# Kernel tuning notes

Hardware: AMD Instinct MI355X
Metric: run time of the kernel (lower is better)

The kernel has to match this reference:

```python
import math
import jax, jax.numpy as jnp
import numpy as np

H, W = 720, 1280
N_GRIDS = 7
CTX = 24          # ARM context pixels
MASK = 9          # causal neighborhood mask size
GAIN = 16.0       # encoder_gain
T = 0.3           # soft_round_temperature
LOG_SCALE_CLAMP = 13.8155
SIZES = [(math.ceil(H / 2 ** i), math.ceil(W / 2 ** i)) for i in range(N_GRIDS)]


def _ctx_offsets():
    # CTX closest strictly-causal pixels (raster order before center) in a 9x9 mask
    c = MASK // 2
    cand = []
    for idx in range((MASK * MASK) // 2):  # indices 0..39 are causal
        r, col = divmod(idx, MASK)
        cand.append(((r - c) ** 2 + (col - c) ** 2, idx, r, col))
    cand.sort()
    sel = sorted(cand[:CTX], key=lambda t: t[1])
    return [(r, col) for _, _, r, col in sel]

OFFSETS = _ctx_offsets()


def softround(x, t):
    fl = jnp.floor(x)
    delta = x - fl - 0.5
    return fl + 0.5 * jnp.tanh(delta / t) / jnp.tanh(0.5 / t) + 0.5


def laplace_cdf(x, mu, scale):
    d = x - mu
    return 0.5 - 0.5 * jnp.sign(d) * jnp.expm1(-jnp.abs(d) / scale)


def get_neighbor(lat):
    # lat: (1,1,h,w) -> (h*w, CTX) causal context, zero padded borders
    h, w = lat.shape[2], lat.shape[3]
    pad = MASK // 2
    p = jnp.pad(lat[0, 0], pad)
    ctx = jnp.stack([p[r:r + h, c:c + w] for (r, c) in OFFSETS], axis=-1)
    return ctx.reshape(-1, CTX)


def depthwise_conv_same(x, k):
    # x: (1,C,h,w), k: (kh,kw) shared across channels
    ch = x.shape[1]
    xr = x.reshape(ch, 1, x.shape[2], x.shape[3])
    y = jax.lax.conv_general_dilated(xr, k[None, None], (1, 1), 'SAME',
                                     dimension_numbers=('NCHW', 'OIHW', 'NCHW'))
    return y.reshape(1, ch, y.shape[2], y.shape[3])


def depthwise_convT2(x, k):
    # stride-2 transposed conv, kernel (8,8) shared across channels
    ch = x.shape[1]
    xr = x.reshape(ch, 1, x.shape[2], x.shape[3])
    y = jax.lax.conv_transpose(xr, k[None, None], (2, 2), 'VALID',
                               dimension_numbers=('NCHW', 'OIHW', 'NCHW'))
    return y.reshape(1, ch, y.shape[2], y.shape[3])


def conv2d(x, w, b):
    y = jax.lax.conv_general_dilated(x, w, (1, 1), 'SAME',
                                     dimension_numbers=('NCHW', 'OIHW', 'NCHW'))
    return y + b[None, :, None, None]


def setup_inputs() -> dict:
    key = jax.random.key(0)
    ks = jax.random.split(key, 24)
    inp = {}
    for i, (h, w) in enumerate(SIZES):
        inp[f'latent{i}'] = jax.random.normal(ks[i], (1, 1, h, w), jnp.float32) * 0.05
    s = 1.0 / math.sqrt(CTX)
    inp['arm_w0'] = jax.random.normal(ks[7], (CTX, 24), jnp.float32) * s
    inp['arm_b0'] = jnp.zeros((24,), jnp.float32)
    inp['arm_w1'] = jax.random.normal(ks[8], (24, 24), jnp.float32) * s
    inp['arm_b1'] = jnp.zeros((24,), jnp.float32)
    inp['arm_wout'] = jax.random.normal(ks[9], (24, 2), jnp.float32) * s
    inp['arm_bout'] = jnp.zeros((2,), jnp.float32)
    inp['pre_kernels'] = jax.random.normal(ks[10], (N_GRIDS - 1, 7, 7), jnp.float32) * 0.05 + \
        jnp.zeros((N_GRIDS - 1, 7, 7), jnp.float32).at[:, 3, 3].set(1.0)
    inp['ups_kernels'] = jax.random.normal(ks[11], (N_GRIDS - 1, 8, 8), jnp.float32) * 0.05 + 0.25
    inp['syn_w0'] = jax.random.normal(ks[12], (48, 7, 1, 1), jnp.float32) * (1.0 / math.sqrt(7))
    inp['syn_b0'] = jnp.zeros((48,), jnp.float32)
    inp['syn_w1'] = jax.random.normal(ks[13], (6, 48, 1, 1), jnp.float32) * (1.0 / math.sqrt(48))
    inp['syn_b1'] = jnp.zeros((6,), jnp.float32)
    inp['syn_w2'] = jax.random.normal(ks[14], (6, 6, 3, 3), jnp.float32) * (1.0 / math.sqrt(54))
    inp['syn_b2'] = jnp.zeros((6,), jnp.float32)
    inp['syn_w3'] = jax.random.normal(ks[15], (6, 6, 3, 3), jnp.float32) * (1.0 / math.sqrt(54))
    inp['syn_b3'] = jnp.zeros((6,), jnp.float32)
    return inp


def _forward(latent0, latent1, latent2, latent3, latent4, latent5, latent6,
             arm_w0, arm_b0, arm_w1, arm_b1, arm_wout, arm_bout,
             pre_kernels, ups_kernels,
             syn_w0, syn_b0, syn_w1, syn_b1, syn_w2, syn_b2, syn_w3, syn_b3):
    lats = [latent0, latent1, latent2, latent3, latent4, latent5, latent6]
    # --- quantize (softround, deterministic) ---
    flat = jnp.concatenate([l.reshape(-1) for l in lats]) * GAIN
    q = softround(flat, T)
    dec, cnt = [], 0
    for l in lats:
        n = l.size
        dec.append(q[cnt:cnt + n].reshape(l.shape))
        cnt += n
    # --- causal neighbor gather + tiny ARM MLP ---
    ctx = jnp.concatenate([get_neighbor(d) for d in dec], axis=0)   # (N, CTX)
    flat_lat = jnp.concatenate([d.reshape(-1) for d in dec])        # (N,)
    h0 = jax.nn.relu(ctx @ arm_w0 + arm_b0)
    h1 = jax.nn.relu(h0 @ arm_w1 + arm_b1)
    out = h1 @ arm_wout + arm_bout                                  # (N, 2)
    mu_f = out[:, 0]
    scale_f = jnp.exp(-0.5 * jnp.clip(out[:, 1], -LOG_SCALE_CLAMP, LOG_SCALE_CLAMP))
    # --- Laplace-CDF rate ---
    proba = jnp.clip(laplace_cdf(flat_lat + 0.5, mu_f, scale_f)
                     - laplace_cdf(flat_lat - 0.5, mu_f, scale_f), 2.0 ** -16, None)
    rate = -jnp.log2(proba)
    # --- upsampling: coarsest -> finest, smooth + x2 transpose conv + concat ---
    x = dec[-1]
    for step, i in enumerate(range(N_GRIDS - 2, -1, -1)):
        x = depthwise_conv_same(x, pre_kernels[step])
        x = depthwise_convT2(x, ups_kernels[step])
        ht, wt = SIZES[i]
        x = x[:, :, 3:3 + ht, 3:3 + wt]
        x = jnp.concatenate([dec[i], x], axis=1)
    # --- synthesis: 48-1-linear-relu, 6-1-linear-none, 6-3-residual-relu, 6-3-residual-none ---
    s0 = jax.nn.relu(conv2d(x, syn_w0, syn_b0))
    s1 = conv2d(s0, syn_w1, syn_b1)
    s2 = jax.nn.relu(conv2d(s1, syn_w2, syn_b2) + s1)
    s3 = conv2d(s2, syn_w3, syn_b3) + s2
    mu = s3[:, :3]
    scale = jnp.exp(-0.5 * jnp.clip(s3[:, 3:6], -LOG_SCALE_CLAMP, LOG_SCALE_CLAMP))
    latent_bpd = rate.sum() / (H * W * 3)
    return mu, scale, rate, latent_bpd


def reference(latent0, latent1, latent2, latent3, latent4, latent5, latent6,
              arm_w0, arm_b0, arm_w1, arm_b1, arm_wout, arm_bout,
              pre_kernels, ups_kernels,
              syn_w0, syn_b0, syn_w1, syn_b1, syn_w2, syn_b2, syn_w3, syn_b3):
    return _forward(latent0, latent1, latent2, latent3, latent4, latent5, latent6,
                    arm_w0, arm_b0, arm_w1, arm_b1, arm_wout, arm_bout,
                    pre_kernels, ups_kernels,
                    syn_w0, syn_b0, syn_w1, syn_b1, syn_w2, syn_b2, syn_w3, syn_b3)
```

## Files before the change

### kernel.cpp

```cpp
#include <hip/hip_runtime.h>

#define NLAT 1228760
#define RATE_OFF 5529600
#define BPD_OFF 6758360
#define NB_ARM 4800
#define LSC 13.8155f

typedef float v2f __attribute__((ext_vector_type(2)));

static __device__ const int d_GOFF[8] = {0,921600,1152000,1209600,1224000,1227600,1228520,1228760};
static __device__ const int d_GW[7]   = {1280,640,320,160,80,40,20};
static __device__ const int d_XOFF[7] = {0,6451200,7833600,8121600,8179200,8190000,8191840};

#define S1_OFF   9574480
#define BSUM_OFF 15104080

static __device__ const int d_DR[24] = {-4,-3,-3,-3,-3,-3,-2,-2,-2,-2,-2,-2,-2,-1,-1,-1,-1,-1,-1,-1, 0, 0, 0, 0};
static __device__ const int d_DC[24] = { 0,-2,-1, 0, 1, 2,-3,-2,-1, 0, 1, 2, 3,-3,-2,-1, 0, 1, 2, 3,-4,-3,-2,-1};

__device__ __forceinline__ float softround_f(float x) {
    float fl = floorf(x);
    float d = x - fl - 0.5f;
    float t = __expf(d * 6.6666667f);
    float th = __fdividef(t - 1.0f, t + 1.0f);
    return fl + 0.5f + 0.53699369f * th;
}

__global__ __launch_bounds__(256) void k_quant(
    const float* __restrict__ l0, const float* __restrict__ l1,
    const float* __restrict__ l2, const float* __restrict__ l3,
    const float* __restrict__ l4, const float* __restrict__ l5,
    const float* __restrict__ l6, float* __restrict__ ws)
{
    int t = blockIdx.x*256 + threadIdx.x;
    if (t >= NLAT) return;
    int g = 0;
    #pragma unroll
    for (int i = 1; i < 7; ++i) if (t >= d_GOFF[i]) g = i;
    int local = t - d_GOFF[g];
    const float* lp = l0;
    if      (g==1) lp=l1; else if (g==2) lp=l2; else if (g==3) lp=l3;
    else if (g==4) lp=l4; else if (g==5) lp=l5; else if (g==6) lp=l6;
    ws[d_XOFF[g] + local] = softround_f(lp[local] * 16.0f);
}

__device__ __forceinline__ void arm_body(
    const float* __restrict__ ws,
    const float* __restrict__ w0, const float* __restrict__ b0,
    const float* __restrict__ w1, const float* __restrict__ b1,
    const float* __restrict__ wo, const float* __restrict__ bo,
    float* __restrict__ out_rate, float* __restrict__ bsum, int ablk)
{
    int t = ablk*256 + threadIdx.x;
    float rate = 0.0f;
    if (t < NLAT) {
        int g = 0;
        #pragma unroll
        for (int i = 1; i < 7; ++i) if (t >= d_GOFF[i]) g = i;
        int local = t - d_GOFF[g];
        int w = d_GW[g];
        int y = (int)((unsigned)local / (unsigned)w);
        int x = local - y*w;
        const float* __restrict__ q = ws + d_XOFF[g];

        float ctx[24];
        if (y >= 4 && x >= 4 && x < w-4) {
            const float* base = q + y*w + x;
            #pragma unroll
            for (int k = 0; k < 24; ++k)
                ctx[k] = base[d_DR[k]*w + d_DC[k]];
        } else {
            #pragma unroll
            for (int k = 0; k < 24; ++k) {
                int yy = y + d_DR[k];
                int xx = x + d_DC[k];
                float v = 0.0f;
                if (yy >= 0 && (unsigned)xx < (unsigned)w) v = q[yy*w + xx];
                ctx[k] = v;
            }
        }

        const v2f* __restrict__ w0v = (const v2f*)w0;
        const v2f* __restrict__ w1v = (const v2f*)w1;
        const v2f* __restrict__ b0v = (const v2f*)b0;
        const v2f* __restrict__ b1v = (const v2f*)b1;
        const v2f* __restrict__ wov = (const v2f*)wo;
        const v2f z2 = {0.0f, 0.0f};

        v2f h0[12];
        #pragma unroll
        for (int j = 0; j < 12; ++j) h0[j] = b0v[j];
        #pragma unroll
        for (int k = 0; k < 24; ++k) {
            v2f c = {ctx[k], ctx[k]};
            #pragma unroll
            for (int j = 0; j < 12; ++j)
                h0[j] = __builtin_elementwise_fma(c, w0v[k*12+j], h0[j]);
        }
        #pragma unroll
        for (int j = 0; j < 12; ++j) h0[j] = __builtin_elementwise_max(h0[j], z2);

        v2f h1[12];
        #pragma unroll
        for (int j = 0; j < 12; ++j) h1[j] = b1v[j];
        #pragma unroll
        for (int k = 0; k < 24; ++k) {
            float hk = h0[k>>1][k&1];
            v2f c = {hk, hk};
            #pragma unroll
            for (int j = 0; j < 12; ++j)
                h1[j] = __builtin_elementwise_fma(c, w1v[k*12+j], h1[j]);
        }
        #pragma unroll
        for (int j = 0; j < 12; ++j) h1[j] = __builtin_elementwise_max(h1[j], z2);

        v2f o = {bo[0], bo[1]};
        #pragma unroll
        for (int j = 0; j < 24; ++j) {
            float hj = h1[j>>1][j&1];
            v2f hh = {hj, hj};
            o = __builtin_elementwise_fma(hh, wov[j], o);
        }

        float mu = o[0];
        float ls = fminf(fmaxf(o[1], -LSC), LSC);
        float inv_s = __expf(0.5f * ls);

        float xv = q[y*w + x];
        float a = xv + 0.5f - mu;
        float b = xv - 0.5f - mu;
        float ka = __expf(-fabsf(a) * inv_s);
        float kb = __expf(-fabsf(b) * inv_s);
        float sa = copysignf(1.0f, a);
        float sb = copysignf(1.0f, b);
        float proba = 0.5f * (sb*(kb - 1.0f) - sa*(ka - 1.0f));
        proba = fmaxf(proba, 1.52587890625e-05f);
        rate = -__log2f(proba);
        out_rate[t] = rate;
    }

    __shared__ float sm[256];
    sm[threadIdx.x] = rate;
    __syncthreads();
    #pragma unroll
    for (int st = 128; st > 0; st >>= 1) {
        if (threadIdx.x < st) sm[threadIdx.x] += sm[threadIdx.x + st];
        __syncthreads();
    }
    if (threadIdx.x == 0) bsum[ablk] = sm[0];
}

template<int CH,int H,int W,int HT,int WT>
__global__ __launch_bounds__(256) void k_level(
    const float* __restrict__ src, float* __restrict__ dst,
    const float* __restrict__ k7, const float* __restrict__ k8,
    const float* __restrict__ ws,
    const float* __restrict__ w0, const float* __restrict__ b0,
    const float* __restrict__ w1, const float* __restrict__ b1,
    const float* __restrict__ wo, const float* __restrict__ bo,
    float* __restrict__ out_rate, float* __restrict__ bsum,
    int arm_off, int arm_cnt)
{
    if ((int)blockIdx.x < arm_cnt) {
        arm_body(ws, w0, b0, w1, b1, wo, bo, out_rate, bsum, arm_off + blockIdx.x);
        return;
    }
    constexpr int HB=(HT+1)/2, WB=(WT+1)/2;
    constexpr int TBH=(HB+15)/16, TBW=(WB+15)/16;
    int blk = blockIdx.x - arm_cnt;
    int c   = blk / (TBH*TBW);
    int r2  = blk - c*(TBH*TBW);
    int tpy = r2 / TBW, tpx = r2 - (r2/TBW)*TBW;
    int IR0 = tpy*16 - 5, IC0 = tpx*16 - 5;

    __shared__ float in_t[26*26];
    __shared__ float pre_t[20*24];

    const float* __restrict__ sc = src + c*H*W;
    for (int i = threadIdx.x; i < 676; i += 256) {
        int r = i/26, col = i - (i/26)*26;
        int gy = IR0 + r, gx = IC0 + col;
        in_t[i] = (gy >= 0 && gy < H && gx >= 0 && gx < W) ? sc[gy*W + gx] : 0.0f;
    }
    __syncthreads();

    for (int i = threadIdx.x; i < 400; i += 256) {
        int r = i/20, s = i - (i/20)*20;
        int gy = IR0 + 3 + r, gx = IC0 + 3 + s;
        float acc = 0.0f;
        if (gy >= 0 && gy < H && gx >= 0 && gx < W) {
            #pragma unroll
            for (int a = 0; a < 7; ++a)
                #pragma unroll
                for (int b = 0; b < 7; ++b)
                    acc = fmaf(in_t[(r+a)*26 + (s+b)], k7[a*7+b], acc);
        }
        pre_t[r*24 + s] = acc;
    }
    __syncthreads();

    int ty = threadIdx.x >> 4, tx = threadIdx.x & 15;
    int pb = tpy*16 + ty, qb = tpx*16 + tx;
    if (pb >= HB || qb >= WB) return;
    float* __restrict__ dc = dst + (c+1)*HT*WT;
    #pragma unroll
    for (int pp = 0; pp < 2; ++pp) {
        int p = 2*pb + pp;
        if (p >= HT) break;
        #pragma unroll
        for (int qq = 0; qq < 2; ++qq) {
            int q = 2*qb + qq;
            if (q >= WT) continue;
            float acc = 0.0f;
            #pragma unroll
            for (int t = 0; t < 4; ++t)
                #pragma unroll
                for (int u = 0; u < 4; ++u)
                    acc = fmaf(pre_t[(ty+pp+t)*24 + (tx+qq+u)], k8[(pp+2*t)*8 + (qq+2*u)], acc);
            dc[p*WT + q] = acc;
        }
    }
}

__global__ __launch_bounds__(256) void k_level01(
    const float* __restrict__ src5,
    const float* __restrict__ src6,
    float* __restrict__ dst,
    const float* __restrict__ k7_0, const float* __restrict__ k8_0,
    const float* __restrict__ k7_1, const float* __restrict__ k8_1,
    const float* __restrict__ ws,
    const float* __restrict__ w0, const float* __restrict__ b0,
    const float* __restrict__ w1, const float* __restrict__ b1,
    const float* __restrict__ wo, const float* __restrict__ bo,
    float* __restrict__ out_rate, float* __restrict__ bsum,
    int arm_off, int arm_cnt)
{
    if ((int)blockIdx.x < arm_cnt) {
        arm_body(ws, w0, b0, w1, b1, wo, bo, out_rate, bsum, arm_off + blockIdx.x);
        return;
    }
    int blk = blockIdx.x - arm_cnt;
    int c   = blk / 6;
    int r2  = blk - c*6;
    int tpy = r2 / 3, tpx = r2 - (r2/3)*3;
    int IR0 = tpy*16 - 5, IC0 = tpx*16 - 5;

    __shared__ float lat6[240];
    __shared__ float pre0_t[240];
    __shared__ float in_t[26*26];
    __shared__ float pre_t[20*24];

    for (int i = threadIdx.x; i < 240; i += 256) lat6[i] = src6[i];
    __syncthreads();
    for (int i = threadIdx.x; i < 240; i += 256) {
        int r = i/20, s = i - (i/20)*20;
        float acc = 0.0f;
        #pragma unroll
        for (int a = 0; a < 7; ++a) {
            int rr = r + a - 3;
            if (rr < 0 || rr >= 12) continue;
            #pragma unroll
            for (int b = 0; b < 7; ++b) {
                int ss = s + b - 3;
                if (ss < 0 || ss >= 20) continue;
                acc = fmaf(lat6[rr*20 + ss], k7_0[a*7+b], acc);
            }
        }
        pre0_t[i] = acc;
    }
    __syncthreads();

    for (int i = threadIdx.x; i < 676; i += 256) {
        int r = i/26, col = i - (i/26)*26;
        int p = IR0 + r, q = IC0 + col;
        float v = 0.0f;
        if (p >= 0 && p < 23 && q >= 0 && q < 40) {
            if (c == 0) {
                v = src5[p*40 + q];
            } else {
                int pp = p & 1, qq2 = q & 1;
                float acc = 0.0f;
                #pragma unroll
                for (int t = 0; t < 4; ++t) {
                    int a = pp + 2*t;
                    int i6 = (p + a - 4) / 2;
                    if (i6 < 0 || i6 >= 12) continue;
                    #pragma unroll
                    for (int u = 0; u < 4; ++u) {
                        int b = qq2 + 2*u;
                        int j6 = (q + b - 4) / 2;
                        if (j6 < 0 || j6 >= 20) continue;
                        acc = fmaf(pre0_t[i6*20 + j6], k8_0[a*8 + b], acc);
                    }
                }
                v = acc;
            }
        }
        in_t[i] = v;
    }
    __syncthreads();

    for (int i = threadIdx.x; i < 400; i += 256) {
        int r = i/20, s = i - (i/20)*20;
        int gy = IR0 + 3 + r, gx = IC0 + 3 + s;
        float acc = 0.0f;
        if (gy >= 0 && gy < 23 && gx >= 0 && gx < 40) {
            #pragma unroll
            for (int a = 0; a < 7; ++a)
                #pragma unroll
                for (int b = 0; b < 7; ++b)
                    acc = fmaf(in_t[(r+a)*26 + (s+b)], k7_1[a*7+b], acc);
        }
        pre_t[r*24 + s] = acc;
    }
    __syncthreads();

    int ty = threadIdx.x >> 4, tx = threadIdx.x & 15;
    int pb = tpy*16 + ty, qb = tpx*16 + tx;
    if (pb >= 23 || qb >= 40) return;
    float* __restrict__ dc = dst + (c+1)*45*80;
    #pragma unroll
    for (int pp = 0; pp < 2; ++pp) {
        int p = 2*pb + pp;
        if (p >= 45) break;
        #pragma unroll
        for (int qq = 0; qq < 2; ++qq) {
            int q = 2*qb + qq;
            if (q >= 80) continue;
            float acc = 0.0f;
            #pragma unroll
            for (int t = 0; t < 4; ++t)
                #pragma unroll
                for (int u = 0; u < 4; ++u)
                    acc = fmaf(pre_t[(ty+pp+t)*24 + (tx+qq+u)], k8_1[(pp+2*t)*8 + (qq+2*u)], acc);
            dc[p*80 + q] = acc;
        }
    }
}

__global__ __launch_bounds__(256, 4) void k_lvl6syn(
    const float* __restrict__ src,
    const float* __restrict__ ch0,
    const float* __restrict__ k7, const float* __restrict__ k8,
    const float* __restrict__ w0, const float* __restrict__ b0,
    const float* __restrict__ w1, const float* __restrict__ b1,
    float* __restrict__ s1,
    const float* __restrict__ bsum, float* __restrict__ out_bpd)
{
    constexpr int H=360, W=640;
    if (blockIdx.x == 0) {
        __shared__ float smr[256];
        float s = 0.0f;
        for (int i = threadIdx.x; i < NB_ARM; i += 256) s += bsum[i];
        smr[threadIdx.x] = s;
        __syncthreads();
        #pragma unroll
        for (int st = 128; st > 0; st >>= 1) {
            if (threadIdx.x < st) smr[threadIdx.x] += smr[threadIdx.x + st];
            __syncthreads();
        }
        if (threadIdx.x == 0) out_bpd[0] = smr[0] * (1.0f/2764800.0f);
        __syncthreads();
    }
    int tpy = blockIdx.x / 40, tpx = blockIdx.x - (blockIdx.x/40)*40;
    int IR0 = tpy*8 - 5, IC0 = tpx*16 - 5;

    __shared__ float in_t[6][18*26];
    __shared__ float pre_t[6][12*24];

    for (int i = threadIdx.x; i < 6*468; i += 256) {
        int c = i / 468, r2 = i - c*468;
        int r = r2/26, col = r2 - r*26;
        int gy = IR0 + r, gx = IC0 + col;
        in_t[c][r2] = (gy >= 0 && gy < H && gx >= 0 && gx < W) ? src[c*H*W + gy*W + gx] : 0.0f;
    }
    __syncthreads();

    for (int i = threadIdx.x; i < 6*240; i += 256) {
        int c = i/240, r2 = i - c*240;
        int r = r2/20, s = r2 - r*20;
        int gy = IR0 + 3 + r, gx = IC0 + 3 + s;
        float acc = 0.0f;
        if (gy >= 0 && gy < H && gx >= 0 && gx < W) {
            #pragma unroll
            for (int a = 0; a < 7; ++a)
                #pragma unroll
                for (int b = 0; b < 7; ++b)
                    acc = fmaf(in_t[c][(r+a)*26 + (s+b)], k7[a*7+b], acc);
        }
        pre_t[c][r*24 + s] = acc;
    }
    __syncthreads();

    int tx = threadIdx.x & 15;
    int ty = (threadIdx.x >> 4) & 7;
    int pp = threadIdx.x >> 7;
    int pb = tpy*8 + ty, qb = tpx*16 + tx;

    v2f in2[7];
    #pragma unroll
    for (int c = 0; c < 6; ++c) {
        v2f acc = {0.0f, 0.0f};
        #pragma unroll
        for (int qq = 0; qq < 2; ++qq) {
            float a = 0.0f;
            #pragma unroll
            for (int t = 0; t < 4; ++t)
                #pragma unroll
                for (int uu = 0; uu < 4; ++uu)
                    a = fmaf(pre_t[c][(ty+pp+t)*24 + (tx+qq+uu)], k8[(pp+2*t)*8 + (qq+2*uu)], a);
            acc[qq] = a;
        }
        in2[c+1] = acc;
    }

    int pix00 = (2*pb + pp)*1280 + 2*qb;
    in2[0] = *(const v2f*)&ch0[pix00];

    v2f out2[6];
    #pragma unroll
    for (int j = 0; j < 6; ++j) out2[j] = (v2f){b1[j], b1[j]};

    const v2f z2 = {0.0f, 0.0f};
    for (int o = 0; o < 48; ++o) {
        float b0o = b0[o];
        v2f a2 = {b0o, b0o};
        #pragma unroll
        for (int c = 0; c < 7; ++c) {
            float wc = w0[o*7 + c];
            a2 = __builtin_elementwise_fma(in2[c], (v2f){wc, wc}, a2);
        }
        a2 = __builtin_elementwise_max(a2, z2);
        #pragma unroll
        for (int j = 0; j < 6; ++j) {
            float wj = w1[j*48 + o];
            out2[j] = __builtin_elementwise_fma(a2, (v2f){wj, wj}, out2[j]);
        }
    }

    #pragma unroll
    for (int j = 0; j < 6; ++j)
        *(v2f*)&s1[j*921600 + pix00] = out2[j];
}

__global__ __launch_bounds__(256, 4) void k_s2s3(
    const float* __restrict__ s1,
    const float* __restrict__ w2, const float* __restrict__ b2,
    const float* __restrict__ w3, const float* __restrict__ b3,
    float* __restrict__ out)
{
    int tpy = blockIdx.x / 40, tpx = blockIdx.x - (blockIdx.x/40)*40;
    int R0 = tpy*16, C0 = tpx*32;

    __shared__ float s1t[6][20*36];
    __shared__ float s2t[6][18*36];

    for (int i = threadIdx.x; i < 6*720; i += 256) {
        int c = i/720, r2 = i - c*720;
        int r = r2/36, col = r2 - r*36;
        int gy = R0 - 2 + r, gx = C0 - 2 + col;
        s1t[c][r2] = (gy >= 0 && gy < 720 && gx >= 0 && gx < 1280)
                   ? s1[c*921600 + gy*1280 + gx] : 0.0f;
    }
    __syncthreads();

    for (int i = threadIdx.x; i < 612; i += 256) {
        int r = i/34, col = i - (i/34)*34;
        int gy = R0 - 1 + r, gx = C0 - 1 + col;
        if (gy >= 0 && gy < 720 && gx >= 0 && gx < 1280) {
            float acc[6];
            #pragma unroll
            for (int o = 0; o < 6; ++o) acc[o] = b2[o];
            #pragma unroll
            for (int ci = 0; ci < 6; ++ci)
                #pragma unroll
                for (int dy = 0; dy < 3; ++dy)
                    #pragma unroll
                    for (int dx = 0; dx < 3; ++dx) {
                        float v = s1t[ci][(r+dy)*36 + col + dx];
                        #pragma unroll
                        for (int o = 0; o < 6; ++o)
                            acc[o] = fmaf(v, w2[(o*6 + ci)*9 + dy*3 + dx], acc[o]);
                    }
            #pragma unroll
            for (int o = 0; o < 6; ++o)
                s2t[o][r*36 + col] = fmaxf(acc[o] + s1t[o][(r+1)*36 + col + 1], 0.0f);
        } else {
            #pragma unroll
            for (int o = 0; o < 6; ++o) s2t[o][r*36 + col] = 0.0f;
        }
    }
    __syncthreads();

    int r  = threadIdx.x >> 4;
    int cp = threadIdx.x & 15;
    int gy = R0 + r;
    int pix00 = gy*1280 + C0 + 2*cp;

    v2f acc2[6];
    #pragma unroll
    for (int o = 0; o < 6; ++o) acc2[o] = (v2f){b3[o], b3[o]};
    #pragma unroll
    for (int ci = 0; ci < 6; ++ci)
        #pragma unroll
        for (int dy = 0; dy < 3; ++dy)
            #pragma unroll
            for (int dx = 0; dx < 3; ++dx) {
                int base = (r+dy)*36 + 2*cp + dx;
                v2f v = { s2t[ci][base], s2t[ci][base + 1] };
                float w = w3[(ci)*9 + dy*3 + dx];
                (void)w;
                #pragma unroll
                for (int o = 0; o < 6; ++o) {
                    float wo_ = w3[(o*6 + ci)*9 + dy*3 + dx];
                    acc2[o] = __builtin_elementwise_fma(v, (v2f){wo_, wo_}, acc2[o]);
                }
            }

    #pragma unroll
    for (int o = 0; o < 6; ++o) {
        int ctr = (r+1)*36 + 2*cp + 1;
        v2f res = { s2t[o][ctr], s2t[o][ctr + 1] };
        v2f v = acc2[o] + res;
        if (o < 3) {
            *(v2f*)&out[o*921600 + pix00] = v;
        } else {
            v2f sc;
            float ls0 = fminf(fmaxf(v[0], -LSC), LSC);
            float ls1 = fminf(fmaxf(v[1], -LSC), LSC);
            sc[0] = __expf(-0.5f * ls0);
            sc[1] = __expf(-0.5f * ls1);
            *(v2f*)&out[2764800 + (o-3)*921600 + pix00] = sc;
        }
    }
}

extern "C" void kernel_launch(void* const* d_in, const int* in_sizes, int n_in,
                              void* d_out, int out_size, void* d_ws, size_t ws_size,
                              hipStream_t stream)
{
    const float* lat[7];
    for (int i = 0; i < 7; ++i) lat[i] = (const float*)d_in[i];
    const float* arm_w0  = (const float*)d_in[7];
    const float* arm_b0  = (const float*)d_in[8];
    const float* arm_w1  = (const float*)d_in[9];
    const float* arm_b1  = (const float*)d_in[10];
    const float* arm_wo  = (const float*)d_in[11];
    const float* arm_bo  = (const float*)d_in[12];
    const float* pre_k   = (const float*)d_in[13];
    const float* ups_k   = (const float*)d_in[14];
    const float* syn_w0  = (const float*)d_in[15];
    const float* syn_b0  = (const float*)d_in[16];
    const float* syn_w1  = (const float*)d_in[17];
    const float* syn_b1  = (const float*)d_in[18];
    const float* syn_w2  = (const float*)d_in[19];
    const float* syn_b2  = (const float*)d_in[20];
    const float* syn_w3  = (const float*)d_in[21];
    const float* syn_b3  = (const float*)d_in[22];

    float* out = (float*)d_out;
    float* ws  = (float*)d_ws;
    float* rate = out + RATE_OFF;
    float* bsum = ws + BSUM_OFF;

    k_quant<<<dim3(NB_ARM), dim3(256), 0, stream>>>(
        lat[0],lat[1],lat[2],lat[3],lat[4],lat[5],lat[6], ws);

    #define ARM_ARGS ws, arm_w0, arm_b0, arm_w1, arm_b1, arm_wo, arm_bo, rate, bsum
    k_level01<<<dim3(1200+12), dim3(256), 0, stream>>>(
        ws+8190000, ws+8191840, ws+8179200,
        pre_k+0*49, ups_k+0*64, pre_k+1*49, ups_k+1*64,
        ARM_ARGS, 0, 1200);
    k_level<3,45,80,90,160><<<dim3(1200+45), dim3(256), 0, stream>>>(
        ws+8179200, ws+8121600, pre_k+2*49, ups_k+2*64, ARM_ARGS, 1200, 1200);
    k_level<4,90,160,180,320><<<dim3(1200+240), dim3(256), 0, stream>>>(
        ws+8121600, ws+7833600, pre_k+3*49, ups_k+3*64, ARM_ARGS, 2400, 1200);
    k_level<5,180,320,360,640><<<dim3(1200+1200), dim3(256), 0, stream>>>(
        ws+7833600, ws+6451200, pre_k+4*49, ups_k+4*64, ARM_ARGS, 3600, 1200);
    #undef ARM_ARGS

    k_lvl6syn<<<dim3(1800), dim3(256), 0, stream>>>(
        ws+6451200, ws+0, pre_k+5*49, ups_k+5*64,
        syn_w0, syn_b0, syn_w1, syn_b1, ws + S1_OFF,
        bsum, out + BPD_OFF);

    k_s2s3<<<dim3(1800), dim3(256), 0, stream>>>(
        ws + S1_OFF, syn_w2, syn_b2, syn_w3, syn_b3, out);
}
```

Before: 237.8 us.

## Compute s2 halo directly from global s1 with paired pixels, dropping s1 smem tile

The s2s3 kernel no longer stages the s1 tile (with halo) into shared memory. Each thread now computes two adjacent s2 pixels by reading s1 straight from global memory with vectorized loads, and a separate bounds-checked path handles edge tiles. This removes a shared-memory stage, a barrier and a large LDS allocation, and raises the occupancy hint from 4 to 6. In exchange, overlapping halo reads now go to global memory or cache, and the misaligned v2f loads at odd columns may be slower.

Measured after the change: 291.5 us. +22.6%, slower.

```diff
diff --git a/kernel.cpp b/kernel.cpp
--- a/kernel.cpp
+++ b/kernel.cpp
@@ -443,7 +443,7 @@
         *(v2f*)&s1[j*921600 + pix00] = out2[j];
 }
 
-__global__ __launch_bounds__(256, 4) void k_s2s3(
+__global__ __launch_bounds__(256, 6) void k_s2s3(
     const float* __restrict__ s1,
     const float* __restrict__ w2, const float* __restrict__ b2,
     const float* __restrict__ w3, const float* __restrict__ b3,
@@ -452,42 +452,86 @@
     int tpy = blockIdx.x / 40, tpx = blockIdx.x - (blockIdx.x/40)*40;
     int R0 = tpy*16, C0 = tpx*32;
 
-    __shared__ float s1t[6][20*36];
     __shared__ float s2t[6][18*36];
 
-    for (int i = threadIdx.x; i < 6*720; i += 256) {
-        int c = i/720, r2 = i - c*720;
-        int r = r2/36, col = r2 - r*36;
-        int gy = R0 - 2 + r, gx = C0 - 2 + col;
-        s1t[c][r2] = (gy >= 0 && gy < 720 && gx >= 0 && gx < 1280)
-                   ? s1[c*921600 + gy*1280 + gx] : 0.0f;
-    }
-    __syncthreads();
-
-    for (int i = threadIdx.x; i < 612; i += 256) {
-        int r = i/34, col = i - (i/34)*34;
-        int gy = R0 - 1 + r, gx = C0 - 1 + col;
-        if (gy >= 0 && gy < 720 && gx >= 0 && gx < 1280) {
-            float acc[6];
-            #pragma unroll
-            for (int o = 0; o < 6; ++o) acc[o] = b2[o];
-            #pragma unroll
-            for (int ci = 0; ci < 6; ++ci)
-                #pragma unroll
-                for (int dy = 0; dy < 3; ++dy)
+    bool edge = (tpy == 0) || (tpy == 44) || (tpx == 0) || (tpx == 39);
+
+    for (int i = threadIdx.x; i < 306; i += 256) {
+        int r  = i / 17, c2 = i - (i/17)*17;
+        int gy = R0 - 1 + r;
+        int gx0 = C0 - 1 + 2*c2;
+
+        v2f acc2[6];
+        #pragma unroll
+        for (int o = 0; o < 6; ++o) acc2[o] = (v2f){b2[o], b2[o]};
+        v2f res2[6];
+
+        if (!edge) {
+            #pragma unroll
+            for (int ci = 0; ci < 6; ++ci) {
+                const float* base = s1 + ci*921600 + (gy-1)*1280 + (gx0-1);
+                #pragma unroll
+                for (int dy = 0; dy < 3; ++dy) {
+                    v2f L01 = *(const v2f*)&base[dy*1280];
+                    v2f L23 = *(const v2f*)&base[dy*1280 + 2];
+                    v2f t0 = L01;
+                    v2f t1 = {L01[1], L23[0]};
+                    v2f t2 = L23;
                     #pragma unroll
-                    for (int dx = 0; dx < 3; ++dx) {
-                        float v = s1t[ci][(r+dy)*36 + col + dx];
-                        #pragma unroll
-                        for (int o = 0; o < 6; ++o)
-                            acc[o] = fmaf(v, w2[(o*6 + ci)*9 + dy*3 + dx], acc[o]);
+                    for (int o = 0; o < 6; ++o) {
+                        float wA = w2[(o*6+ci)*9 + dy*3 + 0];
+                        float wB = w2[(o*6+ci)*9 + dy*3 + 1];
+                        float wC = w2[(o*6+ci)*9 + dy*3 + 2];
+                        acc2[o] = __builtin_elementwise_fma(t0, (v2f){wA,wA}, acc2[o]);
+                        acc2[o] = __builtin_elementwise_fma(t1, (v2f){wB,wB}, acc2[o]);
+                        acc2[o] = __builtin_elementwise_fma(t2, (v2f){wC,wC}, acc2[o]);
                     }
-            #pragma unroll
-            for (int o = 0; o < 6; ++o)
-                s2t[o][r*36 + col] = fmaxf(acc[o] + s1t[o][(r+1)*36 + col + 1], 0.0f);
+                    if (dy == 1) res2[ci] = t1;
+                }
+            }
+            int hc = 2*c2;
+            #pragma unroll
+            for (int o = 0; o < 6; ++o) {
+                s2t[o][r*36 + hc]     = fmaxf(acc2[o][0] + res2[o][0], 0.0f);
+                s2t[o][r*36 + hc + 1] = fmaxf(acc2[o][1] + res2[o][1], 0.0f);
+            }
         } else {
             #pragma unroll
-            for (int o = 0; o < 6; ++o) s2t[o][r*36 + col] = 0.0f;
+            for (int ci = 0; ci < 6; ++ci) {
+                const float* pch = s1 + ci*921600;
+                #pragma unroll
+                for (int dy = 0; dy < 3; ++dy) {
+                    int yy = gy - 1 + dy;
+                    bool ry = (yy >= 0) && (yy < 720);
+                    float Lv[4];
+                    #pragma unroll
+                    for (int dx = 0; dx < 4; ++dx) {
+                        int xx = gx0 - 1 + dx;
+                        Lv[dx] = (ry && xx >= 0 && xx < 1280) ? pch[yy*1280 + xx] : 0.0f;
+                    }
+                    v2f t0 = {Lv[0], Lv[1]};
+                    v2f t1 = {Lv[1], Lv[2]};
+                    v2f t2 = {Lv[2], Lv[3]};
+                    #pragma unroll
+                    for (int o = 0; o < 6; ++o) {
+                        float wA = w2[(o*6+ci)*9 + dy*3 + 0];
+                        float wB = w2[(o*6+ci)*9 + dy*3 + 1];
+                        float wC = w2[(o*6+ci)*9 + dy*3 + 2];
+                        acc2[o] = __builtin_elementwise_fma(t0, (v2f){wA,wA}, acc2[o]);
+                        acc2[o] = __builtin_elementwise_fma(t1, (v2f){wB,wB}, acc2[o]);
+                        acc2[o] = __builtin_elementwise_fma(t2, (v2f){wC,wC}, acc2[o]);
+                    }
+                    if (dy == 1) res2[ci] = t1;
+                }
+            }
+            bool v0 = (gy >= 0) && (gy < 720) && (gx0 >= 0) && (gx0 < 1280);
+            bool v1 = (gy >= 0) && (gy < 720) && (gx0+1 >= 0) && (gx0+1 < 1280);
+            int hc = 2*c2;
+            #pragma unroll
+            for (int o = 0; o < 6; ++o) {
+                s2t[o][r*36 + hc]     = v0 ? fmaxf(acc2[o][0] + res2[o][0], 0.0f) : 0.0f;
+                s2t[o][r*36 + hc + 1] = v1 ? fmaxf(acc2[o][1] + res2[o][1], 0.0f) : 0.0f;
+            }
         }
     }
     __syncthreads();
@@ -508,8 +552,6 @@
             for (int dx = 0; dx < 3; ++dx) {
                 int base = (r+dy)*36 + 2*cp + dx;
                 v2f v = { s2t[ci][base], s2t[ci][base + 1] };
-                float w = w3[(ci)*9 + dy*3 + dx];
-                (void)w;
                 #pragma unroll
                 for (int o = 0; o < 6; ++o) {
                     float wo_ = w3[(o*6 + ci)*9 + dy*3 + dx];
```
